# Kernel optimization log

Hardware: AMD Instinct MI355X
Metric: run time of the kernel (lower is better)

## Reference

```python
import jax, jax.numpy as jnp
import numpy as np


def setup_inputs() -> dict:
    key = jax.random.key(0)
    kA, kB = jax.random.split(key)
    B_, m, n, d = 32, 1024, 1024, 128
    A = jax.random.normal(kA, (B_, m, d), dtype=jnp.float32)
    B = jax.random.normal(kB, (B_, n, d), dtype=jnp.float32)
    return {"A": A, "B": B}


def reference(A, B):
    # e[b,i,j] = <A[b,i], B[b,j]>  -- unnormalized alignment scores
    e = jnp.einsum("bmd,bnd->bmn", A, B)
    # beta[b,i] = sum_j softmax_j(e[b,i,:]) * B[b,j]  (hypothesis aligned to premise)
    beta = jnp.einsum("bmn,bnd->bmd", jax.nn.softmax(e, axis=-1), B)
    # alpha[b,j] = sum_i softmax_i(e[b,:,j]) * A[b,i]  (premise aligned to hypothesis)
    alpha = jnp.einsum("bmn,bmd->bnd", jax.nn.softmax(e, axis=1), A)
    return beta, alpha
```

## Files before the change

### kernel.cpp

```cpp
#include <hip/hip_runtime.h>
#include <hip/hip_bf16.h>
#include <stdint.h>

typedef __attribute__((ext_vector_type(4))) float f32x4;
typedef __attribute__((ext_vector_type(8))) _Float16 f16x8;
typedef __attribute__((ext_vector_type(2))) __fp16 fp16x2;

#define NB 32
#define MM 1024
#define DD 128
#define BKV 64
#define NTILE (MM / BKV)
#define LOG2E 1.44269504089f
#define RTHR 6.0f

static constexpr size_t ARR = (size_t)NB * MM * DD;


__device__ __forceinline__ float fexp2(float x) { return __builtin_amdgcn_exp2f(x); }

__device__ __forceinline__ void gl16(const void* g, void* l) {
  __builtin_amdgcn_global_load_lds((const __attribute__((address_space(1))) void*)g,
                                   (__attribute__((address_space(3))) void*)l, 16, 0, 0);
}

__global__ __launch_bounds__(256) void prep_kernel(const float* __restrict__ A,
                                                   const float* __restrict__ B,
                                                   _Float16* __restrict__ ws) {
  const int rt = blockIdx.x;
  const int b  = blockIdx.y;
  const int wh = blockIdx.z;
  const float* __restrict__ src = wh ? B : A;
  _Float16* __restrict__ Xh  = ws + (size_t)wh * ARR;
  _Float16* __restrict__ XTh = ws + 2 * ARR + (size_t)wh * ARR;

  __shared__ __align__(16) _Float16 tile[64][130];
  const int t = threadIdx.x;

#pragma unroll
  for (int it = 0; it < 4; ++it) {
    int id  = it * 256 + t;
    int row = id >> 4;
    int ch  = id & 15;
    int grow = rt * 64 + row;
    const float* p = src + ((size_t)(b * MM + grow) * DD + ch * 8);
    float4 x0 = *(const float4*)p;
    float4 x1 = *(const float4*)(p + 4);
    f16x8 h;
    h[0] = (_Float16)x0.x; h[1] = (_Float16)x0.y; h[2] = (_Float16)x0.z; h[3] = (_Float16)x0.w;
    h[4] = (_Float16)x1.x; h[5] = (_Float16)x1.y; h[6] = (_Float16)x1.z; h[7] = (_Float16)x1.w;
    char* dst = (char*)Xh + (((size_t)(b * MM + grow)) << 8) + ((ch << 4) ^ ((row & 7) << 4));
    *(f16x8*)dst = h;
#pragma unroll
    for (int j = 0; j < 8; ++j) tile[row][ch * 8 + j] = h[j];
  }
  __syncthreads();

#pragma unroll
  for (int it = 0; it < 4; ++it) {
    int id = it * 256 + t;
    int d  = id >> 3;
    int ch = id & 7;
    f16x8 h;
#pragma unroll
    for (int j = 0; j < 8; ++j) {
      int i = ch * 8 + j;
      int s = (i & 0x23) | ((i & 4) << 2) | ((i & 24) >> 1);
      h[j] = tile[s][d];
    }
    char* dst = (char*)XTh + (((size_t)(b * DD + d)) << 11) + (rt << 7)
              + ((ch << 4) ^ ((d & 7) << 4));
    *(f16x8*)dst = h;
  }
}

__global__ __launch_bounds__(256, 2) void attn_kernel(const _Float16* __restrict__ ws,
                                                      float* __restrict__ out) {
  const int g   = blockIdx.x;
  const int x   = g & 7;
  const int t2  = g >> 3;
  const int qt  = t2 & 7;
  const int p   = ((t2 >> 3) << 3) | x;
  const int b   = p & 31;
  const int dir = p >> 5;

  const _Float16* __restrict__ Qh  = ws + (dir ? ARR : 0);
  const _Float16* __restrict__ Kh  = ws + (dir ? 0 : ARR);
  const _Float16* __restrict__ VTh = ws + 2 * ARR + (dir ? 0 : ARR);
  float* __restrict__ outp = out + (size_t)dir * ARR;

  __shared__ __align__(16) char sbuf[2][32768];

  const int tid  = threadIdx.x;
  const int w    = tid >> 6;
  const int lane = tid & 63;
  const int lrow = lane & 15;
  const int lgrp = lane >> 4;

  const int q0 = qt * 128 + w * 32 + lrow;

  f16x8 qf[2][4];
  {
    const int swz = (lrow & 7) << 4;
#pragma unroll
    for (int qb = 0; qb < 2; ++qb) {
      const char* qbase = (const char*)Qh + (((size_t)(b * MM + q0 + qb * 16)) << 8);
#pragma unroll
      for (int kc = 0; kc < 4; ++kc)
        qf[qb][kc] = *(const f16x8*)(qbase + ((kc * 64 + lgrp * 16) ^ swz));
    }
  }

  const int pl  = (lgrp * 16) ^ ((lrow & 3) << 4);
  const int lb6 = (lrow & 4) << 4;
  const int kE = lrow * 256 + pl + lb6;
  const int kO = lrow * 256 + pl + (64 - lb6);
  const int vE = 16384 + lrow * 128 + pl + lb6;
  const int vO = 16384 + lrow * 128 + pl + (64 - lb6);

  const char* ksrc = (const char*)Kh + (((size_t)b * MM) << 8) + (size_t)tid * 16;
  const char* vsrc = (const char*)VTh + (((size_t)b * DD) << 11)
                   + ((size_t)(tid >> 3) << 11) + (size_t)(tid & 7) * 16;

  f32x4 oacc[2][8];
#pragma unroll
  for (int qb = 0; qb < 2; ++qb)
#pragma unroll
    for (int dt = 0; dt < 8; ++dt) oacc[qb][dt] = (f32x4)0.0f;
  float mrun[2] = {-1e30f, -1e30f};
  float lrun[2] = {0.0f, 0.0f};

  {
    char* sb = sbuf[0];
#pragma unroll
    for (int it = 0; it < 4; ++it)
      gl16(ksrc + it * 4096, sb + it * 4096 + tid * 16);
#pragma unroll
    for (int it = 0; it < 4; ++it)
      gl16(vsrc + it * 65536, sb + 16384 + it * 4096 + tid * 16);
  }
  asm volatile("s_waitcnt vmcnt(0)" ::: "memory");
  __syncthreads();

#pragma unroll 1
  for (int t = 0; t < NTILE; ++t) {
    const char* base = sbuf[t & 1];

    if (t + 1 < NTILE) {
      char* sb = sbuf[(t + 1) & 1];
      const char* kp = ksrc + (size_t)(t + 1) * 16384;
      const char* vp = vsrc + (size_t)(t + 1) * 128;
#pragma unroll
      for (int it = 0; it < 4; ++it)
        gl16(kp + it * 4096, sb + it * 4096 + tid * 16);
#pragma unroll
      for (int it = 0; it < 4; ++it)
        gl16(vp + it * 65536, sb + 16384 + it * 4096 + tid * 16);
    }

    f32x4 sc[2][4];
#pragma unroll
    for (int qb = 0; qb < 2; ++qb)
#pragma unroll
      for (int nt = 0; nt < 4; ++nt) sc[qb][nt] = (f32x4)0.0f;
#pragma unroll
    for (int nt = 0; nt < 4; ++nt) {
#pragma unroll
      for (int kc = 0; kc < 4; ++kc) {
        const int off = ((kc & 1) ? kO + (kc - 1) * 64 : kE + kc * 64) + nt * 4096;
        f16x8 kf = *(const f16x8*)(base + off);
        sc[0][nt] = __builtin_amdgcn_mfma_f32_16x16x32_f16(kf, qf[0][kc], sc[0][nt], 0, 0, 0);
        sc[1][nt] = __builtin_amdgcn_mfma_f32_16x16x32_f16(kf, qf[1][kc], sc[1][nt], 0, 0, 0);
      }
    }

    float mx[2];
#pragma unroll
    for (int qb = 0; qb < 2; ++qb) {
      float m0 = fmaxf(fmaxf(sc[qb][0][0], sc[qb][0][1]), fmaxf(sc[qb][0][2], sc[qb][0][3]));
      float m1 = fmaxf(fmaxf(sc[qb][1][0], sc[qb][1][1]), fmaxf(sc[qb][1][2], sc[qb][1][3]));
      float m2 = fmaxf(fmaxf(sc[qb][2][0], sc[qb][2][1]), fmaxf(sc[qb][2][2], sc[qb][2][3]));
      float m3 = fmaxf(fmaxf(sc[qb][3][0], sc[qb][3][1]), fmaxf(sc[qb][3][2], sc[qb][3][3]));
      float m = fmaxf(fmaxf(m0, m1), fmaxf(m2, m3));
      m = fmaxf(m, __shfl_xor(m, 16));
      m = fmaxf(m, __shfl_xor(m, 32));
      mx[qb] = m;
    }
    bool need = (mx[0] > mrun[0] + RTHR) || (mx[1] > mrun[1] + RTHR);
    if (__any(need)) {
#pragma unroll
      for (int qb = 0; qb < 2; ++qb) {
        float mnew = fmaxf(mrun[qb], mx[qb]);
        float scale = fexp2((mrun[qb] - mnew) * LOG2E);
        lrun[qb] *= scale;
#pragma unroll
        for (int dt = 0; dt < 8; ++dt) oacc[qb][dt] *= scale;
        mrun[qb] = mnew;
      }
    }

    f16x8 pf[2][2];
#pragma unroll
    for (int qb = 0; qb < 2; ++qb) {
      union { fp16x2 h[8]; f16x8 v[2]; } u;
      float ps = 0.0f;
      const float mr = mrun[qb];
#pragma unroll
      for (int nt = 0; nt < 4; ++nt) {
        float p0 = fexp2((sc[qb][nt][0] - mr) * LOG2E);
        float p1 = fexp2((sc[qb][nt][1] - mr) * LOG2E);
        float p2 = fexp2((sc[qb][nt][2] - mr) * LOG2E);
        float p3 = fexp2((sc[qb][nt][3] - mr) * LOG2E);
        ps += (p0 + p1) + (p2 + p3);
        u.h[nt * 2 + 0] = __builtin_amdgcn_cvt_pkrtz(p0, p1);
        u.h[nt * 2 + 1] = __builtin_amdgcn_cvt_pkrtz(p2, p3);
      }
      ps += __shfl_xor(ps, 16);
      ps += __shfl_xor(ps, 32);
      lrun[qb] += ps;
      pf[qb][0] = u.v[0];
      pf[qb][1] = u.v[1];
    }

#pragma unroll
    for (int dt = 0; dt < 8; ++dt) {
      f16x8 v0 = *(const f16x8*)(base + vE + dt * 2048);
      f16x8 v1 = *(const f16x8*)(base + vO + dt * 2048);
      oacc[0][dt] = __builtin_amdgcn_mfma_f32_16x16x32_f16(v0, pf[0][0], oacc[0][dt], 0, 0, 0);
      oacc[0][dt] = __builtin_amdgcn_mfma_f32_16x16x32_f16(v1, pf[0][1], oacc[0][dt], 0, 0, 0);
      oacc[1][dt] = __builtin_amdgcn_mfma_f32_16x16x32_f16(v0, pf[1][0], oacc[1][dt], 0, 0, 0);
      oacc[1][dt] = __builtin_amdgcn_mfma_f32_16x16x32_f16(v1, pf[1][1], oacc[1][dt], 0, 0, 0);
    }

    asm volatile("s_waitcnt vmcnt(0)" ::: "memory");
    __syncthreads();
  }

#pragma unroll
  for (int qb = 0; qb < 2; ++qb) {
    float inv = __builtin_amdgcn_rcpf(lrun[qb]);
    float* op = outp + ((size_t)(b * MM + q0 + qb * 16)) * DD + lgrp * 4;
#pragma unroll
    for (int dt = 0; dt < 8; ++dt) {
      f32x4 v = oacc[qb][dt] * inv;
      *(f32x4*)(op + dt * 16) = v;
    }
  }
}

extern "C" void kernel_launch(void* const* d_in, const int* in_sizes, int n_in,
                              void* d_out, int out_size, void* d_ws, size_t ws_size,
                              hipStream_t stream) {
  const float* A = (const float*)d_in[0];
  const float* B = (const float*)d_in[1];
  float* out = (float*)d_out;
  if (ws_size < 4 * ARR * sizeof(_Float16)) return;
  _Float16* ws = (_Float16*)d_ws;

  dim3 blk(256, 1, 1);
  dim3 g1(16, 32, 2);
  prep_kernel<<<g1, blk, 0, stream>>>(A, B, ws);
  dim3 g2(512, 1, 1);
  attn_kernel<<<g2, blk, 0, stream>>>(ws, out);
}
```

Before: 62.31 us.

## Software-pipeline PV MFMAs across tiles and defer softmax cross-lane reductions

Each tile's V fragments are now loaded into registers and its P·V MFMAs are deferred into the next iteration, after the QK^T MFMAs, with a tail step after the loop. This lets the softmax exp work overlap matrix-core work and frees the LDS buffer earlier. The cross-lane max shuffles now run only when a rescale is triggered, and the row-sum shuffles move to the epilogue. The exponent argument is folded into a single fma. The trade-off is about 64 extra VGPRs for the held V fragments, which could lower occupancy or cause spills.

```diff
diff --git a/kernel.cpp b/kernel.cpp
--- a/kernel.cpp
+++ b/kernel.cpp
@@ -130,6 +130,9 @@
   float mrun[2] = {-1e30f, -1e30f};
   float lrun[2] = {0.0f, 0.0f};
 
+  f16x8 vreg[16];
+  f16x8 pf[2][2];
+
   {
     char* sb = sbuf[0];
 #pragma unroll
@@ -174,23 +177,33 @@
       }
     }
 
+    if (t > 0) {
+#pragma unroll
+      for (int dt = 0; dt < 8; ++dt) {
+        oacc[0][dt] = __builtin_amdgcn_mfma_f32_16x16x32_f16(vreg[dt * 2 + 0], pf[0][0], oacc[0][dt], 0, 0, 0);
+        oacc[0][dt] = __builtin_amdgcn_mfma_f32_16x16x32_f16(vreg[dt * 2 + 1], pf[0][1], oacc[0][dt], 0, 0, 0);
+        oacc[1][dt] = __builtin_amdgcn_mfma_f32_16x16x32_f16(vreg[dt * 2 + 0], pf[1][0], oacc[1][dt], 0, 0, 0);
+        oacc[1][dt] = __builtin_amdgcn_mfma_f32_16x16x32_f16(vreg[dt * 2 + 1], pf[1][1], oacc[1][dt], 0, 0, 0);
+      }
+    }
+
     float mx[2];
 #pragma unroll
     for (int qb = 0; qb < 2; ++qb) {
-      float m0 = fmaxf(fmaxf(sc[qb][0][0], sc[qb][0][1]), fmaxf(sc[qb][0][2], sc[qb][0][3]));
-      float m1 = fmaxf(fmaxf(sc[qb][1][0], sc[qb][1][1]), fmaxf(sc[qb][1][2], sc[qb][1][3]));
-      float m2 = fmaxf(fmaxf(sc[qb][2][0], sc[qb][2][1]), fmaxf(sc[qb][2][2], sc[qb][2][3]));
-      float m3 = fmaxf(fmaxf(sc[qb][3][0], sc[qb][3][1]), fmaxf(sc[qb][3][2], sc[qb][3][3]));
-      float m = fmaxf(fmaxf(m0, m1), fmaxf(m2, m3));
-      m = fmaxf(m, __shfl_xor(m, 16));
-      m = fmaxf(m, __shfl_xor(m, 32));
-      mx[qb] = m;
+      float a0 = fmaxf(fmaxf(sc[qb][0][0], sc[qb][0][1]), fmaxf(sc[qb][0][2], sc[qb][0][3]));
+      float a1 = fmaxf(fmaxf(sc[qb][1][0], sc[qb][1][1]), fmaxf(sc[qb][1][2], sc[qb][1][3]));
+      float a2 = fmaxf(fmaxf(sc[qb][2][0], sc[qb][2][1]), fmaxf(sc[qb][2][2], sc[qb][2][3]));
+      float a3 = fmaxf(fmaxf(sc[qb][3][0], sc[qb][3][1]), fmaxf(sc[qb][3][2], sc[qb][3][3]));
+      mx[qb] = fmaxf(fmaxf(a0, a1), fmaxf(a2, a3));
     }
     bool need = (mx[0] > mrun[0] + RTHR) || (mx[1] > mrun[1] + RTHR);
     if (__any(need)) {
 #pragma unroll
       for (int qb = 0; qb < 2; ++qb) {
-        float mnew = fmaxf(mrun[qb], mx[qb]);
+        float cm = mx[qb];
+        cm = fmaxf(cm, __shfl_xor(cm, 16));
+        cm = fmaxf(cm, __shfl_xor(cm, 32));
+        float mnew = fmaxf(mrun[qb], cm);
         float scale = fexp2((mrun[qb] - mnew) * LOG2E);
         lrun[qb] *= scale;
 #pragma unroll
@@ -199,24 +212,21 @@
       }
     }
 
-    f16x8 pf[2][2];
 #pragma unroll
     for (int qb = 0; qb < 2; ++qb) {
       union { fp16x2 h[8]; f16x8 v[2]; } u;
       float ps = 0.0f;
-      const float mr = mrun[qb];
+      const float nml = -mrun[qb] * LOG2E;
 #pragma unroll
       for (int nt = 0; nt < 4; ++nt) {
-        float p0 = fexp2((sc[qb][nt][0] - mr) * LOG2E);
-        float p1 = fexp2((sc[qb][nt][1] - mr) * LOG2E);
-        float p2 = fexp2((sc[qb][nt][2] - mr) * LOG2E);
-        float p3 = fexp2((sc[qb][nt][3] - mr) * LOG2E);
+        float p0 = fexp2(fmaf(sc[qb][nt][0], LOG2E, nml));
+        float p1 = fexp2(fmaf(sc[qb][nt][1], LOG2E, nml));
+        float p2 = fexp2(fmaf(sc[qb][nt][2], LOG2E, nml));
+        float p3 = fexp2(fmaf(sc[qb][nt][3], LOG2E, nml));
         ps += (p0 + p1) + (p2 + p3);
         u.h[nt * 2 + 0] = __builtin_amdgcn_cvt_pkrtz(p0, p1);
         u.h[nt * 2 + 1] = __builtin_amdgcn_cvt_pkrtz(p2, p3);
       }
-      ps += __shfl_xor(ps, 16);
-      ps += __shfl_xor(ps, 32);
       lrun[qb] += ps;
       pf[qb][0] = u.v[0];
       pf[qb][1] = u.v[1];
@@ -224,12 +234,8 @@
 
 #pragma unroll
     for (int dt = 0; dt < 8; ++dt) {
-      f16x8 v0 = *(const f16x8*)(base + vE + dt * 2048);
-      f16x8 v1 = *(const f16x8*)(base + vO + dt * 2048);
-      oacc[0][dt] = __builtin_amdgcn_mfma_f32_16x16x32_f16(v0, pf[0][0], oacc[0][dt], 0, 0, 0);
-      oacc[0][dt] = __builtin_amdgcn_mfma_f32_16x16x32_f16(v1, pf[0][1], oacc[0][dt], 0, 0, 0);
-      oacc[1][dt] = __builtin_amdgcn_mfma_f32_16x16x32_f16(v0, pf[1][0], oacc[1][dt], 0, 0, 0);
-      oacc[1][dt] = __builtin_amdgcn_mfma_f32_16x16x32_f16(v1, pf[1][1], oacc[1][dt], 0, 0, 0);
+      vreg[dt * 2 + 0] = *(const f16x8*)(base + vE + dt * 2048);
+      vreg[dt * 2 + 1] = *(const f16x8*)(base + vO + dt * 2048);
     }
 
     asm volatile("s_waitcnt vmcnt(0)" ::: "memory");
@@ -237,8 +243,19 @@
   }
 
 #pragma unroll
+  for (int dt = 0; dt < 8; ++dt) {
+    oacc[0][dt] = __builtin_amdgcn_mfma_f32_16x16x32_f16(vreg[dt * 2 + 0], pf[0][0], oacc[0][dt], 0, 0, 0);
+    oacc[0][dt] = __builtin_amdgcn_mfma_f32_16x16x32_f16(vreg[dt * 2 + 1], pf[0][1], oacc[0][dt], 0, 0, 0);
+    oacc[1][dt] = __builtin_amdgcn_mfma_f32_16x16x32_f16(vreg[dt * 2 + 0], pf[1][0], oacc[1][dt], 0, 0, 0);
+    oacc[1][dt] = __builtin_amdgcn_mfma_f32_16x16x32_f16(vreg[dt * 2 + 1], pf[1][1], oacc[1][dt], 0, 0, 0);
+  }
+
+#pragma unroll
   for (int qb = 0; qb < 2; ++qb) {
-    float inv = __builtin_amdgcn_rcpf(lrun[qb]);
+    float l = lrun[qb];
+    l += __shfl_xor(l, 16);
+    l += __shfl_xor(l, 32);
+    float inv = __builtin_amdgcn_rcpf(l);
     float* op = outp + ((size_t)(b * MM + q0 + qb * 16)) * DD + lgrp * 4;
 #pragma unroll
     for (int dt = 0; dt < 8; ++dt) {
```

Result: faster. 58.60 us (-6.0%).

## Load V directly to registers in MFMA layout, use 8 waves of 16 query rows

Applied to the files above, without the earlier changes.

The prep kernel writes V^T pre-permuted into the MFMA operand layout, so the attention kernel can load V fragments straight from global memory into registers instead of staging them through LDS. Each block now runs 512 threads, with each wave handling 16 query rows instead of 32. This halves LDS use and register accumulators per wave, defers the row-sum shuffle to the end, and adds setprio around the MFMA sections. The cost is that every wave reads V from global or L2 redundantly instead of sharing it through LDS, and each wave reuses every K fragment for half as many MFMAs.

```diff
diff --git a/kernel.cpp b/kernel.cpp
--- a/kernel.cpp
+++ b/kernel.cpp
@@ -32,7 +32,7 @@
   const int wh = blockIdx.z;
   const float* __restrict__ src = wh ? B : A;
   _Float16* __restrict__ Xh  = ws + (size_t)wh * ARR;
-  _Float16* __restrict__ XTh = ws + 2 * ARR + (size_t)wh * ARR;
+  _Float16* __restrict__ Vpl = ws + 2 * ARR + (size_t)wh * ARR;
 
   __shared__ __align__(16) _Float16 tile[64][130];
   const int t = threadIdx.x;
@@ -68,13 +68,15 @@
       int s = (i & 0x23) | ((i & 4) << 2) | ((i & 24) >> 1);
       h[j] = tile[s][d];
     }
-    char* dst = (char*)XTh + (((size_t)(b * DD + d)) << 11) + (rt << 7)
-              + ((ch << 4) ^ ((d & 7) << 4));
+    int dt = d >> 4, r = d & 15;
+    int kc2 = ch >> 2, gq = ch & 3;
+    char* dst = (char*)Vpl + (((size_t)(b * 16 + rt)) << 14)
+              + (size_t)(dt * 2 + kc2) * 1024 + (size_t)(gq * 16 + r) * 16;
     *(f16x8*)dst = h;
   }
 }
 
-__global__ __launch_bounds__(256, 2) void attn_kernel(const _Float16* __restrict__ ws,
+__global__ __launch_bounds__(512, 2) void attn_kernel(const _Float16* __restrict__ ws,
                                                       float* __restrict__ out) {
   const int g   = blockIdx.x;
   const int x   = g & 7;
@@ -86,10 +88,10 @@
 
   const _Float16* __restrict__ Qh  = ws + (dir ? ARR : 0);
   const _Float16* __restrict__ Kh  = ws + (dir ? 0 : ARR);
-  const _Float16* __restrict__ VTh = ws + 2 * ARR + (dir ? 0 : ARR);
+  const _Float16* __restrict__ Vpl = ws + 2 * ARR + (dir ? 0 : ARR);
   float* __restrict__ outp = out + (size_t)dir * ARR;
 
-  __shared__ __align__(16) char sbuf[2][32768];
+  __shared__ __align__(16) char sbuf[2][16384];
 
   const int tid  = threadIdx.x;
   const int w    = tid >> 6;
@@ -97,48 +99,32 @@
   const int lrow = lane & 15;
   const int lgrp = lane >> 4;
 
-  const int q0 = qt * 128 + w * 32 + lrow;
-
-  f16x8 qf[2][4];
+  const int q0 = qt * 128 + w * 16 + lrow;
+
+  f16x8 qf[4];
   {
     const int swz = (lrow & 7) << 4;
-#pragma unroll
-    for (int qb = 0; qb < 2; ++qb) {
-      const char* qbase = (const char*)Qh + (((size_t)(b * MM + q0 + qb * 16)) << 8);
-#pragma unroll
-      for (int kc = 0; kc < 4; ++kc)
-        qf[qb][kc] = *(const f16x8*)(qbase + ((kc * 64 + lgrp * 16) ^ swz));
-    }
+    const char* qbase = (const char*)Qh + (((size_t)(b * MM + q0)) << 8);
+#pragma unroll
+    for (int kc = 0; kc < 4; ++kc)
+      qf[kc] = *(const f16x8*)(qbase + ((kc * 64 + lgrp * 16) ^ swz));
   }
 
   const int pl  = (lgrp * 16) ^ ((lrow & 3) << 4);
   const int lb6 = (lrow & 4) << 4;
   const int kE = lrow * 256 + pl + lb6;
   const int kO = lrow * 256 + pl + (64 - lb6);
-  const int vE = 16384 + lrow * 128 + pl + lb6;
-  const int vO = 16384 + lrow * 128 + pl + (64 - lb6);
 
   const char* ksrc = (const char*)Kh + (((size_t)b * MM) << 8) + (size_t)tid * 16;
-  const char* vsrc = (const char*)VTh + (((size_t)b * DD) << 11)
-                   + ((size_t)(tid >> 3) << 11) + (size_t)(tid & 7) * 16;
-
-  f32x4 oacc[2][8];
-#pragma unroll
-  for (int qb = 0; qb < 2; ++qb)
-#pragma unroll
-    for (int dt = 0; dt < 8; ++dt) oacc[qb][dt] = (f32x4)0.0f;
-  float mrun[2] = {-1e30f, -1e30f};
-  float lrun[2] = {0.0f, 0.0f};
-
-  {
-    char* sb = sbuf[0];
-#pragma unroll
-    for (int it = 0; it < 4; ++it)
-      gl16(ksrc + it * 4096, sb + it * 4096 + tid * 16);
-#pragma unroll
-    for (int it = 0; it < 4; ++it)
-      gl16(vsrc + it * 65536, sb + 16384 + it * 4096 + tid * 16);
-  }
+  const char* vtb  = (const char*)Vpl + ((size_t)b << 18) + (size_t)lane * 16;
+
+  f32x4 oacc[8];
+#pragma unroll
+  for (int dt = 0; dt < 8; ++dt) oacc[dt] = (f32x4)0.0f;
+  float mrun = -1e30f, lrun = 0.0f;
+
+  gl16(ksrc, sbuf[0] + tid * 16);
+  gl16(ksrc + 8192, sbuf[0] + 8192 + tid * 16);
   asm volatile("s_waitcnt vmcnt(0)" ::: "memory");
   __syncthreads();
 
@@ -149,102 +135,93 @@
     if (t + 1 < NTILE) {
       char* sb = sbuf[(t + 1) & 1];
       const char* kp = ksrc + (size_t)(t + 1) * 16384;
-      const char* vp = vsrc + (size_t)(t + 1) * 128;
-#pragma unroll
-      for (int it = 0; it < 4; ++it)
-        gl16(kp + it * 4096, sb + it * 4096 + tid * 16);
-#pragma unroll
-      for (int it = 0; it < 4; ++it)
-        gl16(vp + it * 65536, sb + 16384 + it * 4096 + tid * 16);
-    }
-
-    f32x4 sc[2][4];
-#pragma unroll
-    for (int qb = 0; qb < 2; ++qb)
-#pragma unroll
-      for (int nt = 0; nt < 4; ++nt) sc[qb][nt] = (f32x4)0.0f;
+      gl16(kp, sb + tid * 16);
+      gl16(kp + 8192, sb + 8192 + tid * 16);
+    }
+
+    f32x4 sc[4];
+#pragma unroll
+    for (int nt = 0; nt < 4; ++nt) sc[nt] = (f32x4)0.0f;
+    __builtin_amdgcn_s_setprio(1);
 #pragma unroll
     for (int nt = 0; nt < 4; ++nt) {
 #pragma unroll
       for (int kc = 0; kc < 4; ++kc) {
         const int off = ((kc & 1) ? kO + (kc - 1) * 64 : kE + kc * 64) + nt * 4096;
         f16x8 kf = *(const f16x8*)(base + off);
-        sc[0][nt] = __builtin_amdgcn_mfma_f32_16x16x32_f16(kf, qf[0][kc], sc[0][nt], 0, 0, 0);
-        sc[1][nt] = __builtin_amdgcn_mfma_f32_16x16x32_f16(kf, qf[1][kc], sc[1][nt], 0, 0, 0);
+        sc[nt] = __builtin_amdgcn_mfma_f32_16x16x32_f16(kf, qf[kc], sc[nt], 0, 0, 0);
       }
     }
-
-    float mx[2];
-#pragma unroll
-    for (int qb = 0; qb < 2; ++qb) {
-      float m0 = fmaxf(fmaxf(sc[qb][0][0], sc[qb][0][1]), fmaxf(sc[qb][0][2], sc[qb][0][3]));
-      float m1 = fmaxf(fmaxf(sc[qb][1][0], sc[qb][1][1]), fmaxf(sc[qb][1][2], sc[qb][1][3]));
-      float m2 = fmaxf(fmaxf(sc[qb][2][0], sc[qb][2][1]), fmaxf(sc[qb][2][2], sc[qb][2][3]));
-      float m3 = fmaxf(fmaxf(sc[qb][3][0], sc[qb][3][1]), fmaxf(sc[qb][3][2], sc[qb][3][3]));
-      float m = fmaxf(fmaxf(m0, m1), fmaxf(m2, m3));
-      m = fmaxf(m, __shfl_xor(m, 16));
-      m = fmaxf(m, __shfl_xor(m, 32));
-      mx[qb] = m;
-    }
-    bool need = (mx[0] > mrun[0] + RTHR) || (mx[1] > mrun[1] + RTHR);
-    if (__any(need)) {
-#pragma unroll
-      for (int qb = 0; qb < 2; ++qb) {
-        float mnew = fmaxf(mrun[qb], mx[qb]);
-        float scale = fexp2((mrun[qb] - mnew) * LOG2E);
-        lrun[qb] *= scale;
-#pragma unroll
-        for (int dt = 0; dt < 8; ++dt) oacc[qb][dt] *= scale;
-        mrun[qb] = mnew;
+    __builtin_amdgcn_s_setprio(0);
+
+    f16x8 vreg[16];
+    const char* vt = vtb + (size_t)t * 16384;
+#pragma unroll
+    for (int j = 0; j < 8; ++j) vreg[j] = *(const f16x8*)(vt + j * 1024);
+
+    {
+      float a0 = fmaxf(fmaxf(sc[0][0], sc[0][1]), fmaxf(sc[0][2], sc[0][3]));
+      float a1 = fmaxf(fmaxf(sc[1][0], sc[1][1]), fmaxf(sc[1][2], sc[1][3]));
+      float a2 = fmaxf(fmaxf(sc[2][0], sc[2][1]), fmaxf(sc[2][2], sc[2][3]));
+      float a3 = fmaxf(fmaxf(sc[3][0], sc[3][1]), fmaxf(sc[3][2], sc[3][3]));
+      float mx = fmaxf(fmaxf(a0, a1), fmaxf(a2, a3));
+      if (__any(mx > mrun + RTHR)) {
+        float cm = mx;
+        cm = fmaxf(cm, __shfl_xor(cm, 16));
+        cm = fmaxf(cm, __shfl_xor(cm, 32));
+        float mnew = fmaxf(mrun, cm);
+        float scale = fexp2((mrun - mnew) * LOG2E);
+        lrun *= scale;
+#pragma unroll
+        for (int dt = 0; dt < 8; ++dt) oacc[dt] *= scale;
+        mrun = mnew;
       }
     }
 
-    f16x8 pf[2][2];
-#pragma unroll
-    for (int qb = 0; qb < 2; ++qb) {
+    f16x8 pf[2];
+    {
       union { fp16x2 h[8]; f16x8 v[2]; } u;
       float ps = 0.0f;
-      const float mr = mrun[qb];
+      const float nml = -mrun * LOG2E;
 #pragma unroll
       for (int nt = 0; nt < 4; ++nt) {
-        float p0 = fexp2((sc[qb][nt][0] - mr) * LOG2E);
-        float p1 = fexp2((sc[qb][nt][1] - mr) * LOG2E);
-        float p2 = fexp2((sc[qb][nt][2] - mr) * LOG2E);
-        float p3 = fexp2((sc[qb][nt][3] - mr) * LOG2E);
+        float p0 = fexp2(fmaf(sc[nt][0], LOG2E, nml));
+        float p1 = fexp2(fmaf(sc[nt][1], LOG2E, nml));
+        float p2 = fexp2(fmaf(sc[nt][2], LOG2E, nml));
+        float p3 = fexp2(fmaf(sc[nt][3], LOG2E, nml));
         ps += (p0 + p1) + (p2 + p3);
         u.h[nt * 2 + 0] = __builtin_amdgcn_cvt_pkrtz(p0, p1);
         u.h[nt * 2 + 1] = __builtin_amdgcn_cvt_pkrtz(p2, p3);
       }
-      ps += __shfl_xor(ps, 16);
-      ps += __shfl_xor(ps, 32);
-      lrun[qb] += ps;
-      pf[qb][0] = u.v[0];
-      pf[qb][1] = u.v[1];
-    }
-
+      lrun += ps;
+      pf[0] = u.v[0];
+      pf[1] = u.v[1];
+    }
+
+#pragma unroll
+    for (int j = 8; j < 16; ++j) vreg[j] = *(const f16x8*)(vt + j * 1024);
+
+    __builtin_amdgcn_s_setprio(1);
 #pragma unroll
     for (int dt = 0; dt < 8; ++dt) {
-      f16x8 v0 = *(const f16x8*)(base + vE + dt * 2048);
-      f16x8 v1 = *(const f16x8*)(base + vO + dt * 2048);
-      oacc[0][dt] = __builtin_amdgcn_mfma_f32_16x16x32_f16(v0, pf[0][0], oacc[0][dt], 0, 0, 0);
-      oacc[0][dt] = __builtin_amdgcn_mfma_f32_16x16x32_f16(v1, pf[0][1], oacc[0][dt], 0, 0, 0);
-      oacc[1][dt] = __builtin_amdgcn_mfma_f32_16x16x32_f16(v0, pf[1][0], oacc[1][dt], 0, 0, 0);
-      oacc[1][dt] = __builtin_amdgcn_mfma_f32_16x16x32_f16(v1, pf[1][1], oacc[1][dt], 0, 0, 0);
-    }
+      oacc[dt] = __builtin_amdgcn_mfma_f32_16x16x32_f16(vreg[dt * 2 + 0], pf[0], oacc[dt], 0, 0, 0);
+      oacc[dt] = __builtin_amdgcn_mfma_f32_16x16x32_f16(vreg[dt * 2 + 1], pf[1], oacc[dt], 0, 0, 0);
+    }
+    __builtin_amdgcn_s_setprio(0);
 
     asm volatile("s_waitcnt vmcnt(0)" ::: "memory");
     __syncthreads();
   }
 
-#pragma unroll
-  for (int qb = 0; qb < 2; ++qb) {
-    float inv = __builtin_amdgcn_rcpf(lrun[qb]);
-    float* op = outp + ((size_t)(b * MM + q0 + qb * 16)) * DD + lgrp * 4;
-#pragma unroll
-    for (int dt = 0; dt < 8; ++dt) {
-      f32x4 v = oacc[qb][dt] * inv;
-      *(f32x4*)(op + dt * 16) = v;
-    }
+  float l = lrun;
+  l += __shfl_xor(l, 16);
+  l += __shfl_xor(l, 32);
+  float inv = __builtin_amdgcn_rcpf(l);
+  float* op = outp + ((size_t)(b * MM + q0)) * DD + lgrp * 4;
+#pragma unroll
+  for (int dt = 0; dt < 8; ++dt) {
+    f32x4 v = oacc[dt] * inv;
+    *(f32x4*)(op + dt * 16) = v;
   }
 }
 
@@ -257,9 +234,8 @@
   if (ws_size < 4 * ARR * sizeof(_Float16)) return;
   _Float16* ws = (_Float16*)d_ws;
 
-  dim3 blk(256, 1, 1);
   dim3 g1(16, 32, 2);
-  prep_kernel<<<g1, blk, 0, stream>>>(A, B, ws);
+  prep_kernel<<<g1, dim3(256, 1, 1), 0, stream>>>(A, B, ws);
   dim3 g2(512, 1, 1);
-  attn_kernel<<<g2, blk, 0, stream>>>(ws, out);
-}
+  attn_kernel<<<g2, dim3(512, 1, 1), 0, stream>>>(ws, out);
+}
```

Result: slower. 84.19 us (+35.1%).
